# Performance work log

Measured on AMD Instinct MI355X. Metric: run time of the kernel, lower is better.

## Reference

```python
import jax, jax.numpy as jnp
import numpy as np

B = 4096      # batch (number of graphs / query nodes)
N = 524288    # total ball nodes (~128 per graph)
H = 128       # hidden_dim


def setup_inputs() -> dict:
    key = jax.random.key(0)
    ks = jax.random.split(key, 12)
    s = 0.05
    return {
        "query": jax.random.normal(ks[0], (B, H), dtype=jnp.float32),
        "ball": jax.random.normal(ks[1], (N, H), dtype=jnp.float32),
        "ball_batch": jnp.sort(jax.random.randint(ks[2], (N,), 0, B, dtype=jnp.int32)),
        # ball_attention: Linear(H, H//2) -> Tanh -> Linear(H//2, 1)
        "attn_w1": jax.random.normal(ks[3], (H, H // 2), dtype=jnp.float32) * s,
        "attn_b1": jnp.zeros((H // 2,), dtype=jnp.float32),
        "attn_w2": jax.random.normal(ks[4], (H // 2, 1), dtype=jnp.float32) * s,
        "attn_b2": jnp.zeros((1,), dtype=jnp.float32),
        # combiner: Linear(2H, H) -> LayerNorm(H) -> GELU
        "comb_w": jax.random.normal(ks[5], (2 * H, H), dtype=jnp.float32) * s,
        "comb_b": jnp.zeros((H,), dtype=jnp.float32),
        "ln_g": jnp.ones((H,), dtype=jnp.float32),
        "ln_b": jnp.zeros((H,), dtype=jnp.float32),
        # boundary head: Linear(H, H//2) -> ReLU -> Linear(H//2, 1)
        "bnd_w1": jax.random.normal(ks[6], (H, H // 2), dtype=jnp.float32) * s,
        "bnd_b1": jnp.zeros((H // 2,), dtype=jnp.float32),
        "bnd_w2": jax.random.normal(ks[7], (H // 2, 1), dtype=jnp.float32) * s,
        "bnd_b2": jnp.zeros((1,), dtype=jnp.float32),
        # wicket head: Linear(H, H//2) -> ReLU -> Linear(H//2, 1)
        "wkt_w1": jax.random.normal(ks[8], (H, H // 2), dtype=jnp.float32) * s,
        "wkt_b1": jnp.zeros((H // 2,), dtype=jnp.float32),
        "wkt_w2": jax.random.normal(ks[9], (H // 2, 1), dtype=jnp.float32) * s,
        "wkt_b2": jnp.zeros((1,), dtype=jnp.float32),
    }


def reference(query, ball, ball_batch, attn_w1, attn_b1, attn_w2, attn_b2,
              comb_w, comb_b, ln_g, ln_b,
              bnd_w1, bnd_b1, bnd_w2, bnd_b2,
              wkt_w1, wkt_b1, wkt_w2, wkt_b2):
    nb = query.shape[0]  # static batch size
    # attention score MLP over ball nodes -> [N]
    scores = (jnp.tanh(ball @ attn_w1 + attn_b1) @ attn_w2 + attn_b2)[:, 0]
    # segment softmax (stable: subtract per-segment max)
    seg_max = jax.ops.segment_max(scores, ball_batch, num_segments=nb)
    e = jnp.exp(scores - seg_max[ball_batch])
    denom = jax.ops.segment_sum(e, ball_batch, num_segments=nb)
    w = e / denom[ball_batch]
    # weighted-sum pooling -> [B, H]
    pooled = jax.ops.segment_sum(w[:, None] * ball, ball_batch, num_segments=nb)
    # concat + combiner: Linear -> LayerNorm -> GELU (exact, torch default)
    h = jnp.concatenate([query, pooled], axis=-1) @ comb_w + comb_b
    mu = jnp.mean(h, axis=-1, keepdims=True)
    var = jnp.mean((h - mu) ** 2, axis=-1, keepdims=True)
    h = (h - mu) / jnp.sqrt(var + 1e-5) * ln_g + ln_b
    h = jax.nn.gelu(h, approximate=False)
    boundary = jax.nn.relu(h @ bnd_w1 + bnd_b1) @ bnd_w2 + bnd_b2
    wicket = jax.nn.relu(h @ wkt_w1 + wkt_b1) @ wkt_w2 + wkt_b2
    return boundary, wicket
```

## Files before the change

### kernel.cpp

```cpp
#include <hip/hip_runtime.h>
#include <math.h>

#define N_NODES 524288
#define BATCH   4096
#define HID     128
#define MAXL    1024

typedef __attribute__((ext_vector_type(8))) short bf16x8;
typedef __attribute__((ext_vector_type(4))) float f32x4;

__device__ __forceinline__ unsigned short f2bf(float f) {
  unsigned int u = __float_as_uint(f);
  u = (u + 0x7FFFu + ((u >> 16) & 1u)) >> 16;
  return (unsigned short)u;
}

__global__ __launch_bounds__(64) void k_score_pool(
    const float* __restrict__ ball, const int* __restrict__ bb,
    const float* __restrict__ w1, const float* __restrict__ b1,
    const float* __restrict__ w2, const float* __restrict__ b2,
    float* __restrict__ pooled, int N)
{
  __shared__ float s_e[MAXL];
  const int lane = threadIdx.x;
  const int m16  = lane & 15;
  const int quad = lane >> 4;
  const int b    = blockIdx.x;

  int lo = 0, hi = N;
  while (lo < hi) { int mid = (lo + hi) >> 1; if (bb[mid] < b) lo = mid + 1; else hi = mid; }
  const int start = lo;
  hi = N;
  while (lo < hi) { int mid = (lo + hi) >> 1; if (bb[mid] < b + 1) lo = mid + 1; else hi = mid; }
  const int end = lo;
  int L = end - start;

  float4* outp = (float4*)(pooled + (size_t)b * HID);
  if (L <= 0) { if (lane < 32) outp[lane] = make_float4(0.f, 0.f, 0.f, 0.f); return; }
  if (L > MAXL) L = MAXL;

  bf16x8 fb[4][4];
  for (int t = 0; t < 4; ++t) {
    const int n = t * 16 + m16;
    for (int s = 0; s < 4; ++s) {
      const int k0 = s * 32 + quad * 8;
      bf16x8 v;
      #pragma unroll
      for (int j = 0; j < 8; ++j) v[j] = (short)f2bf(w1[(k0 + j) * 64 + n]);
      fb[t][s] = v;
    }
  }
  float b1v[4], w2v[4];
  #pragma unroll
  for (int t = 0; t < 4; ++t) { b1v[t] = b1[t*16 + m16]; w2v[t] = w2[t*16 + m16]; }
  const float b2v = b2[0];

  for (int t0 = 0; t0 < L; t0 += 16) {
    int row = start + t0 + m16;
    if (row > N - 1) row = N - 1;
    const float* rowp = ball + (size_t)row * HID + quad * 8;
    f32x4 acc0 = {0.f,0.f,0.f,0.f}, acc1 = {0.f,0.f,0.f,0.f};
    f32x4 acc2 = {0.f,0.f,0.f,0.f}, acc3 = {0.f,0.f,0.f,0.f};
    #pragma unroll
    for (int s = 0; s < 4; ++s) {
      const float4* p = (const float4*)(rowp + s * 32);
      float4 x0 = p[0], x1 = p[1];
      bf16x8 fa;
      fa[0]=(short)f2bf(x0.x); fa[1]=(short)f2bf(x0.y);
      fa[2]=(short)f2bf(x0.z); fa[3]=(short)f2bf(x0.w);
      fa[4]=(short)f2bf(x1.x); fa[5]=(short)f2bf(x1.y);
      fa[6]=(short)f2bf(x1.z); fa[7]=(short)f2bf(x1.w);
      acc0 = __builtin_amdgcn_mfma_f32_16x16x32_bf16(fa, fb[0][s], acc0, 0,0,0);
      acc1 = __builtin_amdgcn_mfma_f32_16x16x32_bf16(fa, fb[1][s], acc1, 0,0,0);
      acc2 = __builtin_amdgcn_mfma_f32_16x16x32_bf16(fa, fb[2][s], acc2, 0,0,0);
      acc3 = __builtin_amdgcn_mfma_f32_16x16x32_bf16(fa, fb[3][s], acc3, 0,0,0);
    }
    #pragma unroll
    for (int r = 0; r < 4; ++r) {
      float p = tanhf(acc0[r] + b1v[0]) * w2v[0]
              + tanhf(acc1[r] + b1v[1]) * w2v[1]
              + tanhf(acc2[r] + b1v[2]) * w2v[2]
              + tanhf(acc3[r] + b1v[3]) * w2v[3];
      p += __shfl_xor(p, 1); p += __shfl_xor(p, 2);
      p += __shfl_xor(p, 4); p += __shfl_xor(p, 8);
      const int idx = t0 + quad * 4 + r;
      if (m16 == 0 && idx < L) s_e[idx] = p + b2v;
    }
  }
  __syncthreads();

  float m = -INFINITY;
  for (int i = lane; i < L; i += 64) m = fmaxf(m, s_e[i]);
  #pragma unroll
  for (int o = 32; o; o >>= 1) m = fmaxf(m, __shfl_xor(m, o));

  float d = 0.f;
  for (int i = lane; i < L; i += 64) { float e = expf(s_e[i] - m); s_e[i] = e; d += e; }
  __syncthreads();
  #pragma unroll
  for (int o = 32; o; o >>= 1) d += __shfl_xor(d, o);
  const float inv = 1.f / d;

  const int lh = lane >> 5;
  const int c4 = lane & 31;
  float4 acc = {0.f, 0.f, 0.f, 0.f};
  int i = start;
  for (; i + 8 <= end; i += 8) {
    #pragma unroll
    for (int u = 0; u < 4; ++u) {
      const int row = i + 2 * u + lh;
      const float w = s_e[row - start];
      const float4 v = ((const float4*)(ball + (size_t)row * HID))[c4];
      acc.x = fmaf(w, v.x, acc.x);
      acc.y = fmaf(w, v.y, acc.y);
      acc.z = fmaf(w, v.z, acc.z);
      acc.w = fmaf(w, v.w, acc.w);
    }
  }
  for (; i + 2 <= end; i += 2) {
    const int row = i + lh;
    const float w = s_e[row - start];
    const float4 v = ((const float4*)(ball + (size_t)row * HID))[c4];
    acc.x = fmaf(w, v.x, acc.x);
    acc.y = fmaf(w, v.y, acc.y);
    acc.z = fmaf(w, v.z, acc.z);
    acc.w = fmaf(w, v.w, acc.w);
  }
  if (i < end && lh == 0) {
    const int row = i;
    const float w = s_e[row - start];
    const float4 v = ((const float4*)(ball + (size_t)row * HID))[c4];
    acc.x = fmaf(w, v.x, acc.x);
    acc.y = fmaf(w, v.y, acc.y);
    acc.z = fmaf(w, v.z, acc.z);
    acc.w = fmaf(w, v.w, acc.w);
  }
  acc.x += __shfl_xor(acc.x, 32);
  acc.y += __shfl_xor(acc.y, 32);
  acc.z += __shfl_xor(acc.z, 32);
  acc.w += __shfl_xor(acc.w, 32);
  if (lh == 0) {
    acc.x *= inv; acc.y *= inv; acc.z *= inv; acc.w *= inv;
    outp[c4] = acc;
  }
}

__global__ __launch_bounds__(128) void k_combine(
    const float* __restrict__ query, const float* __restrict__ pooled,
    const float* __restrict__ cw, const float* __restrict__ cb,
    const float* __restrict__ lg, const float* __restrict__ lb,
    const float* __restrict__ bw1, const float* __restrict__ bb1,
    const float* __restrict__ bw2, const float* __restrict__ bb2,
    const float* __restrict__ ww1, const float* __restrict__ wb1,
    const float* __restrict__ ww2, const float* __restrict__ wb2,
    float* __restrict__ out)
{
  __shared__ float in_lds[256][8];
  __shared__ float h_lds[128][8];
  __shared__ float part[2][2][8];
  const int tid  = threadIdx.x;
  const int row0 = blockIdx.x * 8;

  for (int idx = tid; idx < 2048; idx += 128) {
    const int k = idx >> 3, r = idx & 7;
    float v = (k < 128) ? query[(size_t)(row0 + r) * 128 + k]
                        : pooled[(size_t)(row0 + r) * 128 + (k - 128)];
    in_lds[k][r] = v;
  }
  __syncthreads();

  const int j = tid;
  float acc[8];
  const float cbj = cb[j];
  #pragma unroll
  for (int r = 0; r < 8; ++r) acc[r] = cbj;
  for (int k = 0; k < 256; ++k) {
    const float w = cw[k * 128 + j];
    #pragma unroll
    for (int r = 0; r < 8; ++r) acc[r] = fmaf(in_lds[k][r], w, acc[r]);
  }

  const int wv = tid >> 6, ln = tid & 63;
  #pragma unroll
  for (int r = 0; r < 8; ++r) {
    float v = acc[r], v2 = v * v;
    #pragma unroll
    for (int o = 32; o; o >>= 1) { v += __shfl_xor(v, o); v2 += __shfl_xor(v2, o); }
    if (ln == 0) { part[0][wv][r] = v; part[1][wv][r] = v2; }
  }
  __syncthreads();
  const float gj = lg[j], bj = lb[j];
  #pragma unroll
  for (int r = 0; r < 8; ++r) {
    const float S = part[0][0][r] + part[0][1][r];
    const float Q = part[1][0][r] + part[1][1][r];
    const float mean = S * (1.f / 128.f);
    const float var  = Q * (1.f / 128.f) - mean * mean;
    const float rs   = rsqrtf(var + 1e-5f);
    float x = (acc[r] - mean) * rs * gj + bj;
    x = 0.5f * x * (1.f + erff(x * 0.70710678118654752f));
    h_lds[j][r] = x;
  }
  __syncthreads();

  const float* W1 = wv ? ww1 : bw1;
  const float* B1 = wv ? wb1 : bb1;
  const float* W2 = wv ? ww2 : bw2;
  const float  B2 = wv ? wb2[0] : bb2[0];
  float t[8];
  const float b1l = B1[ln];
  #pragma unroll
  for (int r = 0; r < 8; ++r) t[r] = b1l;
  for (int k = 0; k < 128; ++k) {
    const float w = W1[k * 64 + ln];
    #pragma unroll
    for (int r = 0; r < 8; ++r) t[r] = fmaf(h_lds[k][r], w, t[r]);
  }
  const float w2l = W2[ln];
  #pragma unroll
  for (int r = 0; r < 8; ++r) {
    float o = fmaxf(t[r], 0.f) * w2l;
    #pragma unroll
    for (int m = 32; m; m >>= 1) o += __shfl_xor(o, m);
    if (ln == 0) out[wv * BATCH + row0 + r] = o + B2;
  }
}

extern "C" void kernel_launch(void* const* d_in, const int* in_sizes, int n_in,
                              void* d_out, int out_size, void* d_ws, size_t ws_size,
                              hipStream_t stream)
{
  const float* query = (const float*)d_in[0];
  const float* ball  = (const float*)d_in[1];
  const int*   bb    = (const int*)  d_in[2];
  const float* aw1   = (const float*)d_in[3];
  const float* ab1   = (const float*)d_in[4];
  const float* aw2   = (const float*)d_in[5];
  const float* ab2   = (const float*)d_in[6];
  const float* cw    = (const float*)d_in[7];
  const float* cb    = (const float*)d_in[8];
  const float* lg    = (const float*)d_in[9];
  const float* lbeta = (const float*)d_in[10];
  const float* bw1   = (const float*)d_in[11];
  const float* bb1   = (const float*)d_in[12];
  const float* bw2   = (const float*)d_in[13];
  const float* bb2   = (const float*)d_in[14];
  const float* ww1   = (const float*)d_in[15];
  const float* wb1   = (const float*)d_in[16];
  const float* ww2   = (const float*)d_in[17];
  const float* wb2   = (const float*)d_in[18];

  float* pooled = (float*)d_ws;
  float* out    = (float*)d_out;

  k_score_pool<<<BATCH, 64, 0, stream>>>(ball, bb, aw1, ab1, aw2, ab2, pooled, N_NODES);
  k_combine<<<BATCH / 8, 128, 0, stream>>>(query, pooled, cw, cb, lg, lbeta,
                                           bw1, bb1, bw2, bb2, ww1, wb1, ww2, wb2, out);
}
```

Measured before the change: 482.4 us.

## Precompute segment bounds and split score/pool across four waves per block

Adds a kernel that computes segment start offsets from the sorted batch ids, replacing two binary searches per block. The score/pool kernel now uses 256 threads, with each wave computing one 16-column slice of the attention MLP and partial scores summed in shared memory. Pooling rows and final reductions are also split across the four waves. tanhf, expf and the division are replaced with fast approximations, which adds extra syncs and a small precision change.

```diff
diff --git a/kernel.cpp b/kernel.cpp
--- a/kernel.cpp
+++ b/kernel.cpp
@@ -4,7 +4,7 @@
 #define N_NODES 524288
 #define BATCH   4096
 #define HID     128
-#define MAXL    1024
+#define MAXL    512
 
 typedef __attribute__((ext_vector_type(8))) short bf16x8;
 typedef __attribute__((ext_vector_type(4))) float f32x4;
@@ -15,121 +15,124 @@
   return (unsigned short)u;
 }
 
-__global__ __launch_bounds__(64) void k_score_pool(
-    const float* __restrict__ ball, const int* __restrict__ bb,
+__device__ __forceinline__ float fast_tanh(float x) {
+  float cx = fminf(fmaxf(x, -9.f), 9.f);
+  float e  = __expf(2.f * cx);
+  return (e - 1.f) * __builtin_amdgcn_rcpf(e + 1.f);
+}
+
+__global__ __launch_bounds__(256) void k_bounds(const int* __restrict__ bb,
+                                                int* __restrict__ rs)
+{
+  const int i = blockIdx.x * 256 + threadIdx.x;
+  if (i >= N_NODES) return;
+  const int cur  = bb[i];
+  const int prev = (i == 0) ? -1 : bb[i - 1];
+  for (int b = prev + 1; b <= cur; ++b) rs[b] = i;
+  if (i == N_NODES - 1)
+    for (int b = cur + 1; b <= BATCH; ++b) rs[b] = N_NODES;
+}
+
+__global__ __launch_bounds__(256, 8) void k_score_pool(
+    const float* __restrict__ ball, const int* __restrict__ rs,
     const float* __restrict__ w1, const float* __restrict__ b1,
     const float* __restrict__ w2, const float* __restrict__ b2,
-    float* __restrict__ pooled, int N)
-{
-  __shared__ float s_e[MAXL];
-  const int lane = threadIdx.x;
+    float* __restrict__ pooled)
+{
+  __shared__ float  s_part[4][MAXL];
+  __shared__ float  s_red[4];
+  __shared__ float4 s_red4[3][32];
+
+  const int tid  = threadIdx.x;
+  const int lane = tid & 63;
+  const int wv   = tid >> 6;
   const int m16  = lane & 15;
   const int quad = lane >> 4;
   const int b    = blockIdx.x;
 
-  int lo = 0, hi = N;
-  while (lo < hi) { int mid = (lo + hi) >> 1; if (bb[mid] < b) lo = mid + 1; else hi = mid; }
-  const int start = lo;
-  hi = N;
-  while (lo < hi) { int mid = (lo + hi) >> 1; if (bb[mid] < b + 1) lo = mid + 1; else hi = mid; }
-  const int end = lo;
+  const int start = rs[b];
+  const int end   = rs[b + 1];
   int L = end - start;
 
   float4* outp = (float4*)(pooled + (size_t)b * HID);
-  if (L <= 0) { if (lane < 32) outp[lane] = make_float4(0.f, 0.f, 0.f, 0.f); return; }
+  if (L <= 0) { if (tid < 32) outp[tid] = make_float4(0.f,0.f,0.f,0.f); return; }
   if (L > MAXL) L = MAXL;
 
-  bf16x8 fb[4][4];
-  for (int t = 0; t < 4; ++t) {
-    const int n = t * 16 + m16;
-    for (int s = 0; s < 4; ++s) {
-      const int k0 = s * 32 + quad * 8;
-      bf16x8 v;
-      #pragma unroll
-      for (int j = 0; j < 8; ++j) v[j] = (short)f2bf(w1[(k0 + j) * 64 + n]);
-      fb[t][s] = v;
-    }
-  }
-  float b1v[4], w2v[4];
-  #pragma unroll
-  for (int t = 0; t < 4; ++t) { b1v[t] = b1[t*16 + m16]; w2v[t] = w2[t*16 + m16]; }
-  const float b2v = b2[0];
+  bf16x8 fb[4];
+  const int n = wv * 16 + m16;
+  #pragma unroll
+  for (int s = 0; s < 4; ++s) {
+    const int k0 = s * 32 + quad * 8;
+    bf16x8 v;
+    #pragma unroll
+    for (int j = 0; j < 8; ++j) v[j] = (short)f2bf(w1[(k0 + j) * 64 + n]);
+    fb[s] = v;
+  }
+  const float b1v = b1[n], w2v = w2[n];
 
   for (int t0 = 0; t0 < L; t0 += 16) {
     int row = start + t0 + m16;
-    if (row > N - 1) row = N - 1;
-    const float* rowp = ball + (size_t)row * HID + quad * 8;
-    f32x4 acc0 = {0.f,0.f,0.f,0.f}, acc1 = {0.f,0.f,0.f,0.f};
-    f32x4 acc2 = {0.f,0.f,0.f,0.f}, acc3 = {0.f,0.f,0.f,0.f};
+    if (row >= end) row = end - 1;
+    const float4* rp = (const float4*)(ball + (size_t)row * HID) + quad * 2;
+    f32x4 acc = {0.f, 0.f, 0.f, 0.f};
     #pragma unroll
     for (int s = 0; s < 4; ++s) {
-      const float4* p = (const float4*)(rowp + s * 32);
-      float4 x0 = p[0], x1 = p[1];
+      float4 x0 = rp[s * 8], x1 = rp[s * 8 + 1];
       bf16x8 fa;
       fa[0]=(short)f2bf(x0.x); fa[1]=(short)f2bf(x0.y);
       fa[2]=(short)f2bf(x0.z); fa[3]=(short)f2bf(x0.w);
       fa[4]=(short)f2bf(x1.x); fa[5]=(short)f2bf(x1.y);
       fa[6]=(short)f2bf(x1.z); fa[7]=(short)f2bf(x1.w);
-      acc0 = __builtin_amdgcn_mfma_f32_16x16x32_bf16(fa, fb[0][s], acc0, 0,0,0);
-      acc1 = __builtin_amdgcn_mfma_f32_16x16x32_bf16(fa, fb[1][s], acc1, 0,0,0);
-      acc2 = __builtin_amdgcn_mfma_f32_16x16x32_bf16(fa, fb[2][s], acc2, 0,0,0);
-      acc3 = __builtin_amdgcn_mfma_f32_16x16x32_bf16(fa, fb[3][s], acc3, 0,0,0);
+      acc = __builtin_amdgcn_mfma_f32_16x16x32_bf16(fa, fb[s], acc, 0,0,0);
     }
     #pragma unroll
     for (int r = 0; r < 4; ++r) {
-      float p = tanhf(acc0[r] + b1v[0]) * w2v[0]
-              + tanhf(acc1[r] + b1v[1]) * w2v[1]
-              + tanhf(acc2[r] + b1v[2]) * w2v[2]
-              + tanhf(acc3[r] + b1v[3]) * w2v[3];
+      float p = fast_tanh(acc[r] + b1v) * w2v;
       p += __shfl_xor(p, 1); p += __shfl_xor(p, 2);
       p += __shfl_xor(p, 4); p += __shfl_xor(p, 8);
       const int idx = t0 + quad * 4 + r;
-      if (m16 == 0 && idx < L) s_e[idx] = p + b2v;
+      if (m16 == 0 && idx < L) s_part[wv][idx] = p;
     }
+    __syncthreads();
   }
   __syncthreads();
 
   float m = -INFINITY;
-  for (int i = lane; i < L; i += 64) m = fmaxf(m, s_e[i]);
+  for (int i = lane; i < L; i += 64)
+    m = fmaxf(m, s_part[0][i] + s_part[1][i] + s_part[2][i] + s_part[3][i]);
   #pragma unroll
   for (int o = 32; o; o >>= 1) m = fmaxf(m, __shfl_xor(m, o));
+  __syncthreads();
 
   float d = 0.f;
-  for (int i = lane; i < L; i += 64) { float e = expf(s_e[i] - m); s_e[i] = e; d += e; }
-  __syncthreads();
+  for (int i = wv * 64 + lane; i < L; i += 256) {
+    float e = __expf(s_part[0][i] + s_part[1][i] + s_part[2][i] + s_part[3][i] - m);
+    s_part[0][i] = e;
+    d += e;
+  }
   #pragma unroll
   for (int o = 32; o; o >>= 1) d += __shfl_xor(d, o);
-  const float inv = 1.f / d;
+  if (lane == 0) s_red[wv] = d;
+  __syncthreads();
+  const float inv = __builtin_amdgcn_rcpf(s_red[0] + s_red[1] + s_red[2] + s_red[3]);
 
   const int lh = lane >> 5;
   const int c4 = lane & 31;
   float4 acc = {0.f, 0.f, 0.f, 0.f};
-  int i = start;
-  for (; i + 8 <= end; i += 8) {
-    #pragma unroll
-    for (int u = 0; u < 4; ++u) {
-      const int row = i + 2 * u + lh;
-      const float w = s_e[row - start];
-      const float4 v = ((const float4*)(ball + (size_t)row * HID))[c4];
-      acc.x = fmaf(w, v.x, acc.x);
-      acc.y = fmaf(w, v.y, acc.y);
-      acc.z = fmaf(w, v.z, acc.z);
-      acc.w = fmaf(w, v.w, acc.w);
-    }
-  }
-  for (; i + 2 <= end; i += 2) {
-    const int row = i + lh;
-    const float w = s_e[row - start];
-    const float4 v = ((const float4*)(ball + (size_t)row * HID))[c4];
+  #pragma unroll 4
+  for (int i = start + wv * 2; i + 1 < end; i += 8) {
+    const int   row = i + lh;
+    const float w   = s_part[0][row - start];
+    const float4 v  = ((const float4*)(ball + (size_t)row * HID))[c4];
     acc.x = fmaf(w, v.x, acc.x);
     acc.y = fmaf(w, v.y, acc.y);
     acc.z = fmaf(w, v.z, acc.z);
     acc.w = fmaf(w, v.w, acc.w);
   }
-  if (i < end && lh == 0) {
-    const int row = i;
-    const float w = s_e[row - start];
-    const float4 v = ((const float4*)(ball + (size_t)row * HID))[c4];
+  if ((L & 1) && wv == 0 && lh == 0) {
+    const int   row = end - 1;
+    const float w   = s_part[0][row - start];
+    const float4 v  = ((const float4*)(ball + (size_t)row * HID))[c4];
     acc.x = fmaf(w, v.x, acc.x);
     acc.y = fmaf(w, v.y, acc.y);
     acc.z = fmaf(w, v.z, acc.z);
@@ -139,9 +142,16 @@
   acc.y += __shfl_xor(acc.y, 32);
   acc.z += __shfl_xor(acc.z, 32);
   acc.w += __shfl_xor(acc.w, 32);
-  if (lh == 0) {
-    acc.x *= inv; acc.y *= inv; acc.z *= inv; acc.w *= inv;
-    outp[c4] = acc;
+  if (wv != 0) { if (lh == 0) s_red4[wv - 1][c4] = acc; }
+  __syncthreads();
+  if (wv == 0 && lh == 0) {
+    const float4 a1 = s_red4[0][c4], a2 = s_red4[1][c4], a3 = s_red4[2][c4];
+    float4 o;
+    o.x = (acc.x + a1.x + a2.x + a3.x) * inv;
+    o.y = (acc.y + a1.y + a2.y + a3.y) * inv;
+    o.z = (acc.z + a1.z + a2.z + a3.z) * inv;
+    o.w = (acc.w + a1.w + a2.w + a3.w) * inv;
+    outp[c4] = o;
   }
 }
 
@@ -251,9 +261,11 @@
   const float* wb2   = (const float*)d_in[18];
 
   float* pooled = (float*)d_ws;
+  int*   rs     = (int*)(pooled + (size_t)BATCH * HID);
   float* out    = (float*)d_out;
 
-  k_score_pool<<<BATCH, 64, 0, stream>>>(ball, bb, aw1, ab1, aw2, ab2, pooled, N_NODES);
+  k_bounds<<<(N_NODES + 255) / 256, 256, 0, stream>>>(bb, rs);
+  k_score_pool<<<BATCH, 256, 0, stream>>>(ball, rs, aw1, ab1, aw2, ab2, pooled);
   k_combine<<<BATCH / 8, 128, 0, stream>>>(query, pooled, cw, cb, lg, lbeta,
                                            bw1, bb1, bw2, bb2, ww1, wb1, ww2, wb2, out);
 }
```

Result: no change. 488.2 us (+1.2%).
